# Performance work log

Hardware: AMD Instinct MI355X
Metric: run time of the kernel (lower is better)

Reference implementation:

```python
import jax, jax.numpy as jnp
import numpy as np

MAX_DISP = 48


def setup_inputs() -> dict:
    key = jax.random.key(0)
    k1, k2 = jax.random.split(key)
    n, c, h, w = 2, 32, 136, 240
    left = jax.random.normal(k1, (n, c, h, w), dtype=jnp.float32)
    right = jax.random.normal(k2, (n, c, h, w), dtype=jnp.float32)
    return {"left": left, "right": right}


def _cost_volume(left, right, max_disp):
    # volume[n, c, d, h, w] = left[n,c,h,w] * right[n,c,h,w-d] for w >= d, else 0
    w = left.shape[-1]
    slices = []
    for d in range(max_disp):
        # shift right feature map by d along W, zero-padding on the left;
        # the zero pad makes volume[..., :d] zero automatically, matching the
        # torch loop that only writes volume[:, :, d, :, d:].
        shifted = jnp.pad(right, ((0, 0), (0, 0), (0, 0), (d, 0)))[..., :w]
        slices.append(left * shifted)
    return jnp.stack(slices, axis=2)  # N x C x D x H x W


def reference(left, right):
    return _cost_volume(left, right, MAX_DISP)
```

## Files before the change

### kernel.cpp

```cpp
#include <hip/hip_runtime.h>


constexpr int W   = 240;
constexpr int H   = 136;
constexpr int D   = 48;
constexpr int W4  = W / 4;
constexpr int DW4 = D * W4;

typedef float v4f __attribute__((ext_vector_type(4)));

__global__ __launch_bounds__(256) void cost_volume_kernel(
    const float* __restrict__ left,
    const float* __restrict__ right,
    float* __restrict__ out)
{
    __shared__ float sL[W];
    __shared__ float sR[D + W];

    const int h   = blockIdx.x;
    const int nc  = blockIdx.y;
    const int tid = threadIdx.x;
    const size_t row = (size_t)(nc * H + h) * W;

    if (tid < W4) {
        reinterpret_cast<v4f*>(sL)[tid] =
            reinterpret_cast<const v4f*>(left + row)[tid];
    } else if (tid >= 64 && tid < 64 + D / 4) {
        reinterpret_cast<v4f*>(sR)[tid - 64] = (v4f){0.f, 0.f, 0.f, 0.f};
    } else if (tid >= 128 && tid < 128 + W4) {
        reinterpret_cast<v4f*>(sR + D)[tid - 128] =
            reinterpret_cast<const v4f*>(right + row)[tid - 128];
    }
    __syncthreads();

    v4f* out4 = reinterpret_cast<v4f*>(out) + ((size_t)nc * D * H + h) * W4 * 1;
    out4 = reinterpret_cast<v4f*>(out) + ((size_t)nc * D * H + h) * (size_t)W4;
    const size_t dstride4 = (size_t)H * W4;
    const float* rpad = sR + D;

    #pragma unroll 2
    for (int i = tid; i < DW4; i += 256) {
        const int d  = i / W4;
        const int w4 = i - d * W4;
        const int w  = w4 * 4;
        const v4f l = reinterpret_cast<const v4f*>(sL)[w4];
        v4f v;
        v.x = l.x * rpad[w + 0 - d];
        v.y = l.y * rpad[w + 1 - d];
        v.z = l.z * rpad[w + 2 - d];
        v.w = l.w * rpad[w + 3 - d];
        __builtin_nontemporal_store(v, &out4[(size_t)d * dstride4 + w4]);
    }
}

extern "C" void kernel_launch(void* const* d_in, const int* in_sizes, int n_in,
                              void* d_out, int out_size, void* d_ws, size_t ws_size,
                              hipStream_t stream) {
    const float* left  = (const float*)d_in[0];
    const float* right = (const float*)d_in[1];
    float* out = (float*)d_out;
    const int rows = in_sizes[0] / W;
    const int nc   = rows / H;
    dim3 grid(H, nc);
    cost_volume_kernel<<<grid, 256, 0, stream>>>(left, right, out);
}
```

Baseline: 412.7 us.

## Use four pre-shifted right-row copies in LDS for aligned vector reads

The kernel now stores four copies of the zero-padded right row in shared memory, each shifted by one element, so every disparity reads an aligned float4 instead of four scalar LDS loads. Each wave handles a fixed group of 12 disparities with the left row kept in registers, and the per-element div/mod indexing goes away. The LDS fill now uses scalar global loads with branches, and lanes 60-63 of each wave sit idle. The kernel is bound by output writes, so the compute savings may barely show.

```diff
diff --git a/kernel.cpp b/kernel.cpp
--- a/kernel.cpp
+++ b/kernel.cpp
@@ -1,11 +1,13 @@
 #include <hip/hip_runtime.h>
 
 
-constexpr int W   = 240;
-constexpr int H   = 136;
-constexpr int D   = 48;
-constexpr int W4  = W / 4;
-constexpr int DW4 = D * W4;
+constexpr int W    = 240;
+constexpr int H    = 136;
+constexpr int D    = 48;
+constexpr int W4   = W / 4;
+constexpr int PAD  = D;
+constexpr int PAD4 = PAD / 4;
+constexpr int CLEN = PAD + W;
 
 typedef float v4f __attribute__((ext_vector_type(4)));
 
@@ -14,42 +16,51 @@
     const float* __restrict__ right,
     float* __restrict__ out)
 {
-    __shared__ float sL[W];
-    __shared__ float sR[D + W];
+    __shared__ __align__(16) float sC[4][CLEN];
 
-    const int h   = blockIdx.x;
-    const int nc  = blockIdx.y;
-    const int tid = threadIdx.x;
+    const int h    = blockIdx.x;
+    const int nc   = blockIdx.y;
+    const int tid  = threadIdx.x;
+    const int wave = tid >> 6;
+    const int lane = tid & 63;
     const size_t row = (size_t)(nc * H + h) * W;
 
-    if (tid < W4) {
-        reinterpret_cast<v4f*>(sL)[tid] =
-            reinterpret_cast<const v4f*>(left + row)[tid];
-    } else if (tid >= 64 && tid < 64 + D / 4) {
-        reinterpret_cast<v4f*>(sR)[tid - 64] = (v4f){0.f, 0.f, 0.f, 0.f};
-    } else if (tid >= 128 && tid < 128 + W4) {
-        reinterpret_cast<v4f*>(sR + D)[tid - 128] =
-            reinterpret_cast<const v4f*>(right + row)[tid - 128];
+    v4f l4 = (v4f){0.f, 0.f, 0.f, 0.f};
+    if (lane < W4) l4 = reinterpret_cast<const v4f*>(left + row)[lane];
+
+    for (int y = tid; y < 4 * CLEN; y += 256) {
+        const int j = y / CLEN;
+        const int x = y - j * CLEN;
+        const int r = x - PAD - j;
+        sC[j][x] = (r >= 0) ? right[row + r] : 0.0f;
     }
     __syncthreads();
 
-    v4f* out4 = reinterpret_cast<v4f*>(out) + ((size_t)nc * D * H + h) * W4 * 1;
-    out4 = reinterpret_cast<v4f*>(out) + ((size_t)nc * D * H + h) * (size_t)W4;
-    const size_t dstride4 = (size_t)H * W4;
-    const float* rpad = sR + D;
+    if (lane >= W4) return;
 
-    #pragma unroll 2
-    for (int i = tid; i < DW4; i += 256) {
-        const int d  = i / W4;
-        const int w4 = i - d * W4;
-        const int w  = w4 * 4;
-        const v4f l = reinterpret_cast<const v4f*>(sL)[w4];
-        v4f v;
-        v.x = l.x * rpad[w + 0 - d];
-        v.y = l.y * rpad[w + 1 - d];
-        v.z = l.z * rpad[w + 2 - d];
-        v.w = l.w * rpad[w + 3 - d];
-        __builtin_nontemporal_store(v, &out4[(size_t)d * dstride4 + w4]);
+    const v4f* C0 = reinterpret_cast<const v4f*>(sC[0]);
+    const v4f* C1 = reinterpret_cast<const v4f*>(sC[1]);
+    const v4f* C2 = reinterpret_cast<const v4f*>(sC[2]);
+    const v4f* C3 = reinterpret_cast<const v4f*>(sC[3]);
+
+    const int d0 = wave * (D / 4);
+    v4f* out4 = reinterpret_cast<v4f*>(out)
+              + (((size_t)nc * D + d0) * H + h) * (size_t)W4 + lane;
+    const size_t ds4 = (size_t)H * W4;
+
+    #pragma unroll
+    for (int tt = 0; tt < 3; ++tt) {
+        const int q    = 3 * wave + tt;
+        const int base = PAD4 + lane - q;
+        const v4f r0 = C0[base];
+        const v4f r1 = C1[base];
+        const v4f r2 = C2[base];
+        const v4f r3 = C3[base];
+        v4f* o = out4 + (size_t)(4 * tt) * ds4;
+        __builtin_nontemporal_store(l4 * r0, o);
+        __builtin_nontemporal_store(l4 * r1, o + ds4);
+        __builtin_nontemporal_store(l4 * r2, o + 2 * ds4);
+        __builtin_nontemporal_store(l4 * r3, o + 3 * ds4);
     }
 }
 
```

New measurement: 411.5 us. Within noise of the previous version (-0.3%).

## Assign one block per disparity plane and read inputs directly from global memory

Applied to the files above, without the earlier changes.

Changes the grid from one block per (row, channel) to one block per (disparity, channel). Each block writes a contiguous H*W output plane and reads left and right straight from global memory, relying on cache reuse instead of shared memory staging and a barrier. It also replaces the nontemporal stores with ordinary stores. In exchange, inputs are re-read once per disparity, which depends on L2 hit rates, and the unaligned scalar right loads are less efficient.

```diff
diff --git a/kernel.cpp b/kernel.cpp
--- a/kernel.cpp
+++ b/kernel.cpp
@@ -5,7 +5,7 @@
 constexpr int H   = 136;
 constexpr int D   = 48;
 constexpr int W4  = W / 4;
-constexpr int DW4 = D * W4;
+constexpr int HW4 = H * W4;
 
 typedef float v4f __attribute__((ext_vector_type(4)));
 
@@ -14,42 +14,32 @@
     const float* __restrict__ right,
     float* __restrict__ out)
 {
-    __shared__ float sL[W];
-    __shared__ float sR[D + W];
+    const int d  = blockIdx.x;
+    const int nc = blockIdx.y;
 
-    const int h   = blockIdx.x;
-    const int nc  = blockIdx.y;
-    const int tid = threadIdx.x;
-    const size_t row = (size_t)(nc * H + h) * W;
+    const float* __restrict__ L = left  + (size_t)nc * (H * W);
+    const float* __restrict__ R = right + (size_t)nc * (H * W);
+    v4f* __restrict__ O = reinterpret_cast<v4f*>(out) + ((size_t)nc * D + d) * (size_t)HW4;
 
-    if (tid < W4) {
-        reinterpret_cast<v4f*>(sL)[tid] =
-            reinterpret_cast<const v4f*>(left + row)[tid];
-    } else if (tid >= 64 && tid < 64 + D / 4) {
-        reinterpret_cast<v4f*>(sR)[tid - 64] = (v4f){0.f, 0.f, 0.f, 0.f};
-    } else if (tid >= 128 && tid < 128 + W4) {
-        reinterpret_cast<v4f*>(sR + D)[tid - 128] =
-            reinterpret_cast<const v4f*>(right + row)[tid - 128];
-    }
-    __syncthreads();
+    for (int i = threadIdx.x; i < HW4; i += 256) {
+        const int h   = (unsigned)i / W4;
+        const int w4  = i - h * W4;
+        const int row = h * W;
 
-    v4f* out4 = reinterpret_cast<v4f*>(out) + ((size_t)nc * D * H + h) * W4 * 1;
-    out4 = reinterpret_cast<v4f*>(out) + ((size_t)nc * D * H + h) * (size_t)W4;
-    const size_t dstride4 = (size_t)H * W4;
-    const float* rpad = sR + D;
+        const v4f l = *reinterpret_cast<const v4f*>(L + row + 4 * w4);
 
-    #pragma unroll 2
-    for (int i = tid; i < DW4; i += 256) {
-        const int d  = i / W4;
-        const int w4 = i - d * W4;
-        const int w  = w4 * 4;
-        const v4f l = reinterpret_cast<const v4f*>(sL)[w4];
+        const int off = 4 * w4 - d;
+        const float r0 = R[row + ((off + 0 >= 0) ? off + 0 : 0)];
+        const float r1 = R[row + ((off + 1 >= 0) ? off + 1 : 0)];
+        const float r2 = R[row + ((off + 2 >= 0) ? off + 2 : 0)];
+        const float r3 = R[row + ((off + 3 >= 0) ? off + 3 : 0)];
+
         v4f v;
-        v.x = l.x * rpad[w + 0 - d];
-        v.y = l.y * rpad[w + 1 - d];
-        v.z = l.z * rpad[w + 2 - d];
-        v.w = l.w * rpad[w + 3 - d];
-        __builtin_nontemporal_store(v, &out4[(size_t)d * dstride4 + w4]);
+        v.x = (off + 0 >= 0) ? l.x * r0 : 0.f;
+        v.y = (off + 1 >= 0) ? l.y * r1 : 0.f;
+        v.z = (off + 2 >= 0) ? l.z * r2 : 0.f;
+        v.w = (off + 3 >= 0) ? l.w * r3 : 0.f;
+        O[i] = v;
     }
 }
 
@@ -61,6 +51,6 @@
     float* out = (float*)d_out;
     const int rows = in_sizes[0] / W;
     const int nc   = rows / H;
-    dim3 grid(H, nc);
+    dim3 grid(D, nc);
     cost_volume_kernel<<<grid, 256, 0, stream>>>(left, right, out);
 }
```

After: 510.5 us. +23.7%, slower.
